# Kernel optimization log

Hardware: AMD Instinct MI355X
Metric: run time of the kernel (lower is better)

## Reference

```python
import jax, jax.numpy as jnp
import numpy as np

B, N, D, H = 16, 512, 256, 8
E_PER = 16384  # edges per graph (avg degree 32)
BN_EPS = 1e-5


def _bn(x, g, b, m, v):
    # BatchNorm1d in eval mode: normalize with running stats
    return (x - m) * (g * jax.lax.rsqrt(v + BN_EPS)) + b


def setup_inputs() -> dict:
    key = jax.random.key(0)
    ks = jax.random.split(key, 32)
    E = B * E_PER
    w = lambda k, s: (jax.random.normal(k, s, jnp.float32) * 0.02)
    # block-diagonal edge list: indices within each graph + graph offset
    src = jax.random.randint(ks[1], (B, E_PER), 0, N)
    dst = jax.random.randint(ks[2], (B, E_PER), 0, N)
    off = (jnp.arange(B) * N)[:, None]
    inp = {
        "x": jax.random.normal(ks[0], (B * N, D), jnp.float32),
        "edge_rows": (src + off).reshape(-1).astype(jnp.int32),
        "edge_cols": (dst + off).reshape(-1).astype(jnp.int32),
        "edge_vals": jax.random.uniform(ks[3], (E,), jnp.float32) * 0.1,
        "w_gcn": w(ks[4], (D, D)),
        "in_proj_w": w(ks[5], (3 * D, D)),
        "in_proj_b": w(ks[6], (3 * D,)),
        "out_proj_w": w(ks[7], (D, D)),
        "out_proj_b": w(ks[8], (D,)),
        "w1": w(ks[9], (4 * D, D)),
        "b1": w(ks[10], (4 * D,)),
        "w2": w(ks[11], (D, 4 * D)),
        "b2": w(ks[12], (D,)),
        "batch_size": B,
        "num_nodes": N,
    }
    for i, name in enumerate(["bn1", "bn2", "bn3"]):
        k4 = jax.random.split(ks[13 + i], 4)
        inp[name + "_g"] = 1.0 + jax.random.uniform(k4[0], (D,), jnp.float32) * 0.1
        inp[name + "_b"] = w(k4[1], (D,))
        inp[name + "_m"] = w(k4[2], (D,))
        inp[name + "_v"] = 1.0 + jax.random.uniform(k4[3], (D,), jnp.float32) * 0.1
    return inp


def reference(x, edge_rows, edge_cols, edge_vals, w_gcn,
              in_proj_w, in_proj_b, out_proj_w, out_proj_b,
              bn1_g, bn1_b, bn1_m, bn1_v,
              bn2_g, bn2_b, bn2_m, bn2_v,
              bn3_g, bn3_b, bn3_m, bn3_v,
              w1, b1, w2, b2, batch_size, num_nodes):
    n_total = x.shape[0]
    dh = D // H
    # --- local GCN: linear -> sparse SpMM (gather/scatter) -> exact GELU ---
    hl = x @ w_gcn.T                                            # (BN, D)
    agg = jax.ops.segment_sum(edge_vals[:, None] * hl[edge_cols],
                              edge_rows, num_segments=n_total)   # (BN, D)
    h_local = jax.nn.gelu(agg, approximate=False)
    x = x + h_local
    x = _bn(x, bn1_g, bn1_b, bn1_m, bn1_v)
    # --- global multi-head self-attention per graph ---
    h = x.reshape(batch_size, num_nodes, D)
    qkv = jnp.einsum('bnd,ed->bne', h, in_proj_w) + in_proj_b    # (B, N, 3D)
    q, k, v = jnp.split(qkv, 3, axis=-1)
    q = q.reshape(batch_size, num_nodes, H, dh)
    k = k.reshape(batch_size, num_nodes, H, dh)
    v = v.reshape(batch_size, num_nodes, H, dh)
    scores = jnp.einsum('bqhd,bkhd->bhqk', q, k) / jnp.sqrt(jnp.float32(dh))
    attn = jax.nn.softmax(scores, axis=-1)
    ctx = jnp.einsum('bhqk,bkhd->bqhd', attn, v).reshape(batch_size, num_nodes, D)
    h_attn = (ctx @ out_proj_w.T + out_proj_b).reshape(n_total, D)
    x = x + h_attn
    x = _bn(x, bn2_g, bn2_b, bn2_m, bn2_v)
    # --- FFN ---
    h_ffn = jax.nn.gelu(x @ w1.T + b1, approximate=False) @ w2.T + b2
    x = x + h_ffn
    x = _bn(x, bn3_g, bn3_b, bn3_m, bn3_v)
    return x
```

## Files before the change

### kernel.cpp

```cpp
#include <hip/hip_runtime.h>
#include <hip/hip_bf16.h>
#include <math.h>

#define D_    256
#define NT_   8192
#define NN_   512
#define B_    16
#define H_    8
#define EPG_  16384
#define BN_EPS 1e-5f

typedef __attribute__((ext_vector_type(8))) short bx8;
typedef __attribute__((ext_vector_type(4))) float fx4;

__device__ __forceinline__ float gelu_exact(float x) {
    return 0.5f * x * (1.0f + erff(x * 0.70710678118654752f));
}

typedef __attribute__((address_space(1))) const unsigned int GU;
typedef __attribute__((address_space(3))) unsigned int LU;
__device__ __forceinline__ void gl_lds16(const void* g, void* l) {
    __builtin_amdgcn_global_load_lds((GU*)g, (LU*)l, 16, 0, 0);
}

template<int TM, int TN, int EPI, int OBF, int RBF>
__global__ __launch_bounds__(256)
void mgemm(const short* __restrict__ A, const short* __restrict__ Bw,
           const float* __restrict__ bias, void* __restrict__ Cout,
           int M, int N, int K,
           long sA, long sB, long sC, long sR,
           const void* __restrict__ resid,
           const float* __restrict__ bng, const float* __restrict__ bnb,
           const float* __restrict__ bnm, const float* __restrict__ bnv)
{
    constexpr int MR = TM / 32, NR = TN / 32;
    constexpr int NIA = TM / 8, NIB = TN / 8;
    __shared__ short As[2][TM][64];
    __shared__ short Bs[2][TN][64];
    const int bz = blockIdx.z;
    A  += (size_t)bz * sA;
    Bw += (size_t)bz * sB;
    const int bm = blockIdx.y * TM, bn = blockIdx.x * TN;
    const int tid = threadIdx.x;
    const int w = tid >> 6, lane = tid & 63;
    const int wm = w >> 1, wn = w & 1;
    const int fr = lane & 15;
    const int srow = lane >> 3;
    const int scol = (((lane & 7) ^ (srow & 7)) << 3);
    fx4 acc[MR][NR] = {};

    auto STAGE = [&](int buf, int k0) {
        #pragma unroll
        for (int i = w; i < NIA + NIB; i += 4) {
            if (i < NIA)
                gl_lds16(A + (size_t)(bm + i * 8 + srow) * K + k0 + scol,
                         (char*)&As[buf][0][0] + i * 1024);
            else
                gl_lds16(Bw + (size_t)(bn + (i - NIA) * 8 + srow) * K + k0 + scol,
                         (char*)&Bs[buf][0][0] + (i - NIA) * 1024);
        }
    };

    STAGE(0, 0);
    __syncthreads();
    const int T = K >> 6;
    for (int t = 0; t < T; ++t) {
        const int cur = t & 1;
        if (t + 1 < T) STAGE(cur ^ 1, (t + 1) << 6);
        #pragma unroll
        for (int ks = 0; ks < 2; ++ks) {
            const int sl = (ks << 2) | (lane >> 4);
            bx8 af[MR], bf[NR];
            #pragma unroll
            for (int m = 0; m < MR; ++m) {
                const int row = wm * (TM / 2) + m * 16 + fr;
                af[m] = *(const bx8*)&As[cur][row][(sl ^ (row & 7)) << 3];
            }
            #pragma unroll
            for (int n = 0; n < NR; ++n) {
                const int row = wn * (TN / 2) + n * 16 + fr;
                bf[n] = *(const bx8*)&Bs[cur][row][(sl ^ (row & 7)) << 3];
            }
            #pragma unroll
            for (int m = 0; m < MR; ++m)
                #pragma unroll
                for (int n = 0; n < NR; ++n)
                    acc[m][n] = __builtin_amdgcn_mfma_f32_16x16x32_bf16(af[m], bf[n], acc[m][n], 0, 0, 0);
        }
        __syncthreads();
    }

    float* Cf = (float*)Cout + (size_t)bz * sC;
    __hip_bfloat16* Cb = (__hip_bfloat16*)Cout + (size_t)bz * sC;
    const float* Rf = (const float*)resid + (EPI >= 2 ? (size_t)bz * sR : 0);
    const __hip_bfloat16* Rb = (const __hip_bfloat16*)resid + (EPI >= 2 ? (size_t)bz * sR : 0);
    #pragma unroll
    for (int m = 0; m < MR; ++m) {
        #pragma unroll
        for (int n = 0; n < NR; ++n) {
            #pragma unroll
            for (int r = 0; r < 4; ++r) {
                const int gm = bm + wm * (TM / 2) + m * 16 + (lane >> 4) * 4 + r;
                const int gn = bn + wn * (TN / 2) + n * 16 + fr;
                float v = acc[m][n][r];
                if (bias) v += bias[gn];
                if (EPI == 1) v = gelu_exact(v);
                if (EPI == 2 || EPI == 3) {
                    const float rv = RBF ? __bfloat162float(Rb[(size_t)gm * N + gn])
                                         : Rf[(size_t)gm * N + gn];
                    if (EPI == 2) v += rv;
                    else          v = rv + gelu_exact(v);
                    v = (v - bnm[gn]) * (bng[gn] * rsqrtf(bnv[gn] + BN_EPS)) + bnb[gn];
                }
                if (OBF) Cb[(size_t)gm * N + gn] = __float2bfloat16(v);
                else     Cf[(size_t)gm * N + gn] = v;
            }
        }
    }
}

__device__ __forceinline__ void cv4(const float4 v, __hip_bfloat16* d) {
    __hip_bfloat162* dp = (__hip_bfloat162*)d;
    dp[0] = __hip_bfloat162(__float2bfloat16(v.x), __float2bfloat16(v.y));
    dp[1] = __hip_bfloat162(__float2bfloat16(v.z), __float2bfloat16(v.w));
}

__global__ __launch_bounds__(256)
void conv6(const float* __restrict__ x,  const float* __restrict__ wg,
           const float* __restrict__ iw, const float* __restrict__ ow,
           const float* __restrict__ w1, const float* __restrict__ w2,
           __hip_bfloat16* xb, __hip_bfloat16* wgb, __hip_bfloat16* iwb,
           __hip_bfloat16* owb, __hip_bfloat16* w1b, __hip_bfloat16* w2b)
{
    int i = blockIdx.x * 256 + threadIdx.x;
    const float* s; __hip_bfloat16* d; int o;
    if      (i < 524288) { s = x;  d = xb;  o = i; }
    else if (i < 540672) { s = wg; d = wgb; o = i - 524288; }
    else if (i < 589824) { s = iw; d = iwb; o = i - 540672; }
    else if (i < 606208) { s = ow; d = owb; o = i - 589824; }
    else if (i < 671744) { s = w1; d = w1b; o = i - 606208; }
    else                 { s = w2; d = w2b; o = i - 671744; }
    cv4(((const float4*)s)[o], d + (size_t)o * 4);
}

__global__ __launch_bounds__(256)
void convA(const float* __restrict__ s, __hip_bfloat16* __restrict__ d, int n4)
{
    int i = blockIdx.x * 256 + threadIdx.x;
    if (i >= n4) return;
    cv4(((const float4*)s)[i], d + (size_t)i * 4);
}

__global__ __launch_bounds__(256)
void build_S(const int* __restrict__ rows, const int* __restrict__ cols,
             const float* __restrict__ vals, float* __restrict__ SA)
{
    const int e = blockIdx.x * 256 + threadIdx.x;
    const int r = rows[e], c = cols[e];
    const int g = r >> 9;
    atomicAdd(&SA[((size_t)g << 18) + (size_t)(r & 511) * 512 + (c - (g << 9))], vals[e]);
}

__global__ __launch_bounds__(256)
void transp(const __hip_bfloat16* __restrict__ hl, __hip_bfloat16* __restrict__ hlB)
{
    __shared__ short T[64][72];
    const int nt = blockIdx.x, it = blockIdx.y, g = blockIdx.z;
    const int r0 = threadIdx.x >> 3, c8 = (threadIdx.x & 7) << 3;
    #pragma unroll
    for (int u = 0; u < 2; ++u) {
        const int r = r0 + u * 32;
        *(bx8*)&T[r][c8] = *(const bx8*)&hl[(size_t)(g * 512 + it * 64 + r) * 256 + nt * 64 + c8];
    }
    __syncthreads();
    #pragma unroll
    for (int u = 0; u < 2; ++u) {
        const int r = r0 + u * 32;
        bx8 o;
        #pragma unroll
        for (int j = 0; j < 8; ++j) o[j] = T[c8 + j][r];
        *(bx8*)&hlB[((size_t)(g * 256 + nt * 64 + r)) * 512 + it * 64 + c8] = o;
    }
}

__global__ __launch_bounds__(256, 1)
void attn_mfma(const short* __restrict__ qkv, __hip_bfloat16* __restrict__ ctx)
{
    const int swz = (blockIdx.x & 7) * 128 + (blockIdx.x >> 3);
    const int qt = swz & 7;
    const int h  = (swz >> 3) & 7;
    const int b  = swz >> 6;
    __shared__ short Ks[512][40];
    __shared__ short Vt[32][520];
    __shared__ short Ps[64][520];
    const int tid = threadIdx.x;
    const int lane = tid & 63, wq = tid >> 6;
    const short* base = qkv + (size_t)b * NN_ * 768;

    {
        const int d0 = (tid & 3) << 3;
        const int k0 = tid >> 2;
        #pragma unroll
        for (int rep = 0; rep < 8; ++rep) {
            const int key = k0 + rep * 64;
            *(bx8*)&Ks[key][d0] =
                *(const bx8*)(base + (size_t)key * 768 + 256 + h * 32 + d0);
        }
    }
    {
        const int d0 = (tid >> 6) << 3;
        const int k0 = tid & 63;
        #pragma unroll
        for (int rep = 0; rep < 8; ++rep) {
            const int key = k0 + rep * 64;
            bx8 vv = *(const bx8*)(base + (size_t)key * 768 + 512 + h * 32 + d0);
            #pragma unroll
            for (int j = 0; j < 8; ++j) Vt[d0 + j][key] = vv[j];
        }
    }
    const int fr = lane & 15, fk = (lane >> 4) << 3;
    const int qrow = qt * 64 + wq * 16 + fr;
    bx8 qf = *(const bx8*)(base + (size_t)qrow * 768 + h * 32 + fk);
    __syncthreads();

    fx4 sc[32];
    #pragma unroll
    for (int nt = 0; nt < 32; ++nt) {
        bx8 kf = *(const bx8*)&Ks[nt * 16 + fr][fk];
        fx4 z = {0.f, 0.f, 0.f, 0.f};
        sc[nt] = __builtin_amdgcn_mfma_f32_16x16x32_bf16(qf, kf, z, 0, 0, 0);
    }

    const float scale = 0.17677669529663687f;
    #pragma unroll
    for (int r = 0; r < 4; ++r) {
        float m = -1e30f;
        #pragma unroll
        for (int nt = 0; nt < 32; ++nt) m = fmaxf(m, sc[nt][r]);
        #pragma unroll
        for (int off = 1; off < 16; off <<= 1)
            m = fmaxf(m, __shfl_xor(m, off, 64));
        const float M = m * scale;
        float s = 0.f;
        #pragma unroll
        for (int nt = 0; nt < 32; ++nt) {
            const float p = __expf(sc[nt][r] * scale - M);
            sc[nt][r] = p;
            s += p;
        }
        #pragma unroll
        for (int off = 1; off < 16; off <<= 1) s += __shfl_xor(s, off, 64);
        const float inv = 1.0f / s;
        const int q = wq * 16 + (lane >> 4) * 4 + r;
        #pragma unroll
        for (int nt = 0; nt < 32; ++nt)
            *(__hip_bfloat16*)&Ps[q][nt * 16 + fr] = __float2bfloat16(sc[nt][r] * inv);
    }

    fx4 oacc[2] = {};
    #pragma unroll
    for (int step = 0; step < 16; ++step) {
        bx8 pf = *(const bx8*)&Ps[wq * 16 + fr][step * 32 + fk];
        #pragma unroll
        for (int nt = 0; nt < 2; ++nt) {
            bx8 vf = *(const bx8*)&Vt[nt * 16 + fr][step * 32 + fk];
            oacc[nt] = __builtin_amdgcn_mfma_f32_16x16x32_bf16(pf, vf, oacc[nt], 0, 0, 0);
        }
    }
    #pragma unroll
    for (int nt = 0; nt < 2; ++nt) {
        #pragma unroll
        for (int r = 0; r < 4; ++r) {
            const int q = qt * 64 + wq * 16 + (lane >> 4) * 4 + r;
            const int d = nt * 16 + fr;
            ctx[(size_t)(b * NN_ + q) * D_ + h * 32 + d] = __float2bfloat16(oacc[nt][r]);
        }
    }
}

extern "C" void kernel_launch(void* const* d_in, const int* in_sizes, int n_in,
                              void* d_out, int out_size, void* d_ws, size_t ws_size,
                              hipStream_t stream) {
    const float* x      = (const float*)d_in[0];
    const int*   erows  = (const int*)d_in[1];
    const int*   ecols  = (const int*)d_in[2];
    const float* evals  = (const float*)d_in[3];
    const float* w_gcn  = (const float*)d_in[4];
    const float* in_w   = (const float*)d_in[5];
    const float* in_b   = (const float*)d_in[6];
    const float* outw   = (const float*)d_in[7];
    const float* outb   = (const float*)d_in[8];
    const float* w1     = (const float*)d_in[9];
    const float* b1     = (const float*)d_in[10];
    const float* w2     = (const float*)d_in[11];
    const float* b2     = (const float*)d_in[12];
    const float* bn1g = (const float*)d_in[15], *bn1b = (const float*)d_in[16];
    const float* bn1m = (const float*)d_in[17], *bn1v = (const float*)d_in[18];
    const float* bn2g = (const float*)d_in[19], *bn2b = (const float*)d_in[20];
    const float* bn2m = (const float*)d_in[21], *bn2v = (const float*)d_in[22];
    const float* bn3g = (const float*)d_in[23], *bn3b = (const float*)d_in[24];
    const float* bn3m = (const float*)d_in[25], *bn3v = (const float*)d_in[26];

    short* wsS = (short*)d_ws;
    __hip_bfloat16* xb    = (__hip_bfloat16*)(wsS + 0);
    __hip_bfloat16* wgcnb = (__hip_bfloat16*)(wsS + 2097152);
    __hip_bfloat16* iwb   = (__hip_bfloat16*)(wsS + 2162688);
    __hip_bfloat16* owb   = (__hip_bfloat16*)(wsS + 2359296);
    __hip_bfloat16* w1b   = (__hip_bfloat16*)(wsS + 2424832);
    __hip_bfloat16* w2b   = (__hip_bfloat16*)(wsS + 2686976);
    short* hl   = wsS + 2949120;
    short* hlB  = wsS + 5046272;
    short* x1b  = wsS + 7143424;
    short* ctxb = wsS + 9240576;
    short* x2b  = wsS + 11337728;
    short* h1b  = wsS + 13434880;
    short* SAb  = wsS + 21823488;
    float* SA   = (float*)(wsS + 26017792);
    short* qkvb = wsS + 26017792;
    float* out  = (float*)d_out;

    dim3 blk(256);
    conv6<<<dim3(2880), blk, 0, stream>>>(x, w_gcn, in_w, outw, w1, w2,
                                          xb, wgcnb, iwb, owb, w1b, w2b);
    hipMemsetAsync(SA, 0, (size_t)16 * 512 * 512 * 4, stream);
    build_S<<<dim3(1024), blk, 0, stream>>>(erows, ecols, evals, SA);
    convA<<<dim3(4096), blk, 0, stream>>>(SA, (__hip_bfloat16*)SAb, 1048576);
    mgemm<64,64,0,1,0><<<dim3(4, 128), blk, 0, stream>>>((const short*)xb, (const short*)wgcnb,
        nullptr, hl, NT_, D_, D_, 0,0,0,0, nullptr, nullptr, nullptr, nullptr, nullptr);
    transp<<<dim3(4, 8, 16), blk, 0, stream>>>((const __hip_bfloat16*)hl, (__hip_bfloat16*)hlB);
    mgemm<64,64,3,1,0><<<dim3(4, 8, 16), blk, 0, stream>>>(SAb, hlB, nullptr, x1b,
        512, D_, 512, 262144, 131072, 131072, 131072,
        x, bn1g, bn1b, bn1m, bn1v);
    mgemm<64,64,0,1,0><<<dim3(12, 128), blk, 0, stream>>>(x1b, (const short*)iwb, in_b, qkvb,
        NT_, 3 * D_, D_, 0,0,0,0, nullptr, nullptr, nullptr, nullptr, nullptr);
    attn_mfma<<<dim3(1024), blk, 0, stream>>>(qkvb, (__hip_bfloat16*)ctxb);
    mgemm<64,64,2,1,1><<<dim3(4, 128), blk, 0, stream>>>(ctxb, (const short*)owb, outb, x2b,
        NT_, D_, D_, 0,0,0,0, x1b, bn2g, bn2b, bn2m, bn2v);
    mgemm<64,64,1,1,0><<<dim3(16, 128), blk, 0, stream>>>(x2b, (const short*)w1b, b1, h1b,
        NT_, 4 * D_, D_, 0,0,0,0, nullptr, nullptr, nullptr, nullptr, nullptr);
    mgemm<64,64,2,0,1><<<dim3(4, 128), blk, 0, stream>>>(h1b, (const short*)w2b, b2, out,
        NT_, D_, 4 * D_, 0,0,0,0, x2b, bn3g, bn3b, bn3m, bn3v);
}
```

Baseline: 246.7 us.

## Fuse transposed stores into GEMM epilogues and streamline attention softmax

Adds an EPI==4 GEMM epilogue that writes a column range directly in transposed (per-graph, feature-major) bf16 layout. This removes the separate transpose kernel for the GCN hidden features and also pre-transposes V during the QKV projection. Attention can then load Vt with contiguous vector loads instead of scattered LDS writes. The attention kernel also swaps the MFMA operands so each lane holds one query row, which cuts the softmax shuffle reductions to two steps and lets P be stored as packed 4-element vectors. The cost is strided 8-byte global stores in the GEMM epilogue for the transposed part.

```diff
diff --git a/kernel.cpp b/kernel.cpp
--- a/kernel.cpp
+++ b/kernel.cpp
@@ -11,10 +11,15 @@
 #define BN_EPS 1e-5f
 
 typedef __attribute__((ext_vector_type(8))) short bx8;
+typedef __attribute__((ext_vector_type(4))) short sx4;
 typedef __attribute__((ext_vector_type(4))) float fx4;
 
 __device__ __forceinline__ float gelu_exact(float x) {
     return 0.5f * x * (1.0f + erff(x * 0.70710678118654752f));
+}
+__device__ __forceinline__ short bf16s(float v) {
+    __hip_bfloat16 hb = __float2bfloat16(v);
+    return *(short*)&hb;
 }
 
 typedef __attribute__((address_space(1))) const unsigned int GU;
@@ -92,16 +97,18 @@
 
     float* Cf = (float*)Cout + (size_t)bz * sC;
     __hip_bfloat16* Cb = (__hip_bfloat16*)Cout + (size_t)bz * sC;
-    const float* Rf = (const float*)resid + (EPI >= 2 ? (size_t)bz * sR : 0);
-    const __hip_bfloat16* Rb = (const __hip_bfloat16*)resid + (EPI >= 2 ? (size_t)bz * sR : 0);
+    const float* Rf = (const float*)resid + ((EPI == 2 || EPI == 3) ? (size_t)bz * sR : 0);
+    const __hip_bfloat16* Rb = (const __hip_bfloat16*)resid + ((EPI == 2 || EPI == 3) ? (size_t)bz * sR : 0);
     #pragma unroll
     for (int m = 0; m < MR; ++m) {
         #pragma unroll
         for (int n = 0; n < NR; ++n) {
+            const int gm0 = bm + wm * (TM / 2) + m * 16 + (lane >> 4) * 4;
+            const int gn  = bn + wn * (TN / 2) + n * 16 + fr;
+            float vv[4];
             #pragma unroll
             for (int r = 0; r < 4; ++r) {
-                const int gm = bm + wm * (TM / 2) + m * 16 + (lane >> 4) * 4 + r;
-                const int gn = bn + wn * (TN / 2) + n * 16 + fr;
+                const int gm = gm0 + r;
                 float v = acc[m][n][r];
                 if (bias) v += bias[gn];
                 if (EPI == 1) v = gelu_exact(v);
@@ -112,8 +119,27 @@
                     else          v = rv + gelu_exact(v);
                     v = (v - bnm[gn]) * (bng[gn] * rsqrtf(bnv[gn] + BN_EPS)) + bnb[gn];
                 }
-                if (OBF) Cb[(size_t)gm * N + gn] = __float2bfloat16(v);
-                else     Cf[(size_t)gm * N + gn] = v;
+                vv[r] = v;
+            }
+            if (EPI == 4) {
+                const int tc = (int)sR;
+                if (gn >= tc) {
+                    short* Tout = (short*)resid;
+                    sx4 pk;
+                    #pragma unroll
+                    for (int r = 0; r < 4; ++r) pk[r] = bf16s(vv[r]);
+                    *(sx4*)(Tout + ((size_t)((gm0 >> 9) * (N - tc) + (gn - tc))) * 512 + (gm0 & 511)) = pk;
+                } else {
+                    #pragma unroll
+                    for (int r = 0; r < 4; ++r)
+                        Cb[(size_t)(gm0 + r) * N + gn] = __float2bfloat16(vv[r]);
+                }
+            } else {
+                #pragma unroll
+                for (int r = 0; r < 4; ++r) {
+                    if (OBF) Cb[(size_t)(gm0 + r) * N + gn] = __float2bfloat16(vv[r]);
+                    else     Cf[(size_t)(gm0 + r) * N + gn] = vv[r];
+                }
             }
         }
     }
@@ -161,30 +187,9 @@
     atomicAdd(&SA[((size_t)g << 18) + (size_t)(r & 511) * 512 + (c - (g << 9))], vals[e]);
 }
 
-__global__ __launch_bounds__(256)
-void transp(const __hip_bfloat16* __restrict__ hl, __hip_bfloat16* __restrict__ hlB)
-{
-    __shared__ short T[64][72];
-    const int nt = blockIdx.x, it = blockIdx.y, g = blockIdx.z;
-    const int r0 = threadIdx.x >> 3, c8 = (threadIdx.x & 7) << 3;
-    #pragma unroll
-    for (int u = 0; u < 2; ++u) {
-        const int r = r0 + u * 32;
-        *(bx8*)&T[r][c8] = *(const bx8*)&hl[(size_t)(g * 512 + it * 64 + r) * 256 + nt * 64 + c8];
-    }
-    __syncthreads();
-    #pragma unroll
-    for (int u = 0; u < 2; ++u) {
-        const int r = r0 + u * 32;
-        bx8 o;
-        #pragma unroll
-        for (int j = 0; j < 8; ++j) o[j] = T[c8 + j][r];
-        *(bx8*)&hlB[((size_t)(g * 256 + nt * 64 + r)) * 512 + it * 64 + c8] = o;
-    }
-}
-
 __global__ __launch_bounds__(256, 1)
-void attn_mfma(const short* __restrict__ qkv, __hip_bfloat16* __restrict__ ctx)
+void attn_mfma(const short* __restrict__ qkv, const short* __restrict__ VtG,
+               __hip_bfloat16* __restrict__ ctx)
 {
     const int swz = (blockIdx.x & 7) * 128 + (blockIdx.x >> 3);
     const int qt = swz & 7;
@@ -196,6 +201,7 @@
     const int tid = threadIdx.x;
     const int lane = tid & 63, wq = tid >> 6;
     const short* base = qkv + (size_t)b * NN_ * 768;
+    const short* vtb  = VtG + (size_t)(b * 8 + h) * 32 * 512;
 
     {
         const int d0 = (tid & 3) << 3;
@@ -208,14 +214,11 @@
         }
     }
     {
-        const int d0 = (tid >> 6) << 3;
-        const int k0 = tid & 63;
+        const int d = tid >> 3, c0 = (tid & 7) << 3;
         #pragma unroll
         for (int rep = 0; rep < 8; ++rep) {
-            const int key = k0 + rep * 64;
-            bx8 vv = *(const bx8*)(base + (size_t)key * 768 + 512 + h * 32 + d0);
-            #pragma unroll
-            for (int j = 0; j < 8; ++j) Vt[d0 + j][key] = vv[j];
+            const int c = c0 + rep * 64;
+            *(bx8*)&Vt[d][c] = *(const bx8*)(vtb + (size_t)d * 512 + c);
         }
     }
     const int fr = lane & 15, fk = (lane >> 4) << 3;
@@ -228,33 +231,40 @@
     for (int nt = 0; nt < 32; ++nt) {
         bx8 kf = *(const bx8*)&Ks[nt * 16 + fr][fk];
         fx4 z = {0.f, 0.f, 0.f, 0.f};
-        sc[nt] = __builtin_amdgcn_mfma_f32_16x16x32_bf16(qf, kf, z, 0, 0, 0);
+        sc[nt] = __builtin_amdgcn_mfma_f32_16x16x32_bf16(kf, qf, z, 0, 0, 0);
     }
 
     const float scale = 0.17677669529663687f;
-    #pragma unroll
-    for (int r = 0; r < 4; ++r) {
-        float m = -1e30f;
-        #pragma unroll
-        for (int nt = 0; nt < 32; ++nt) m = fmaxf(m, sc[nt][r]);
-        #pragma unroll
-        for (int off = 1; off < 16; off <<= 1)
-            m = fmaxf(m, __shfl_xor(m, off, 64));
-        const float M = m * scale;
-        float s = 0.f;
-        #pragma unroll
-        for (int nt = 0; nt < 32; ++nt) {
+    float mx = -1e30f;
+    #pragma unroll
+    for (int nt = 0; nt < 32; ++nt)
+        mx = fmaxf(mx, fmaxf(fmaxf(sc[nt][0], sc[nt][1]), fmaxf(sc[nt][2], sc[nt][3])));
+    mx = fmaxf(mx, __shfl_xor(mx, 16, 64));
+    mx = fmaxf(mx, __shfl_xor(mx, 32, 64));
+    const float M = mx * scale;
+    float s = 0.f;
+    #pragma unroll
+    for (int nt = 0; nt < 32; ++nt) {
+        #pragma unroll
+        for (int r = 0; r < 4; ++r) {
             const float p = __expf(sc[nt][r] * scale - M);
             sc[nt][r] = p;
             s += p;
         }
-        #pragma unroll
-        for (int off = 1; off < 16; off <<= 1) s += __shfl_xor(s, off, 64);
-        const float inv = 1.0f / s;
-        const int q = wq * 16 + (lane >> 4) * 4 + r;
-        #pragma unroll
-        for (int nt = 0; nt < 32; ++nt)
-            *(__hip_bfloat16*)&Ps[q][nt * 16 + fr] = __float2bfloat16(sc[nt][r] * inv);
+    }
+    s += __shfl_xor(s, 16, 64);
+    s += __shfl_xor(s, 32, 64);
+    const float inv = 1.0f / s;
+    {
+        const int q = wq * 16 + fr;
+        const int kb = (lane >> 4) << 2;
+        #pragma unroll
+        for (int nt = 0; nt < 32; ++nt) {
+            sx4 pk;
+            #pragma unroll
+            for (int r = 0; r < 4; ++r) pk[r] = bf16s(sc[nt][r] * inv);
+            *(sx4*)&Ps[q][nt * 16 + kb] = pk;
+        }
     }
 
     fx4 oacc[2] = {};
@@ -308,7 +318,7 @@
     __hip_bfloat16* owb   = (__hip_bfloat16*)(wsS + 2359296);
     __hip_bfloat16* w1b   = (__hip_bfloat16*)(wsS + 2424832);
     __hip_bfloat16* w2b   = (__hip_bfloat16*)(wsS + 2686976);
-    short* hl   = wsS + 2949120;
+    short* VtG  = wsS + 2949120;
     short* hlB  = wsS + 5046272;
     short* x1b  = wsS + 7143424;
     short* ctxb = wsS + 9240576;
@@ -325,15 +335,14 @@
     hipMemsetAsync(SA, 0, (size_t)16 * 512 * 512 * 4, stream);
     build_S<<<dim3(1024), blk, 0, stream>>>(erows, ecols, evals, SA);
     convA<<<dim3(4096), blk, 0, stream>>>(SA, (__hip_bfloat16*)SAb, 1048576);
-    mgemm<64,64,0,1,0><<<dim3(4, 128), blk, 0, stream>>>((const short*)xb, (const short*)wgcnb,
-        nullptr, hl, NT_, D_, D_, 0,0,0,0, nullptr, nullptr, nullptr, nullptr, nullptr);
-    transp<<<dim3(4, 8, 16), blk, 0, stream>>>((const __hip_bfloat16*)hl, (__hip_bfloat16*)hlB);
+    mgemm<64,64,4,1,0><<<dim3(4, 128), blk, 0, stream>>>((const short*)xb, (const short*)wgcnb,
+        nullptr, nullptr, NT_, D_, D_, 0,0,0,0, hlB, nullptr, nullptr, nullptr, nullptr);
     mgemm<64,64,3,1,0><<<dim3(4, 8, 16), blk, 0, stream>>>(SAb, hlB, nullptr, x1b,
         512, D_, 512, 262144, 131072, 131072, 131072,
         x, bn1g, bn1b, bn1m, bn1v);
-    mgemm<64,64,0,1,0><<<dim3(12, 128), blk, 0, stream>>>(x1b, (const short*)iwb, in_b, qkvb,
-        NT_, 3 * D_, D_, 0,0,0,0, nullptr, nullptr, nullptr, nullptr, nullptr);
-    attn_mfma<<<dim3(1024), blk, 0, stream>>>(qkvb, (__hip_bfloat16*)ctxb);
+    mgemm<64,64,4,1,0><<<dim3(12, 128), blk, 0, stream>>>(x1b, (const short*)iwb, in_b, qkvb,
+        NT_, 3 * D_, D_, 0,0,0,512, VtG, nullptr, nullptr, nullptr, nullptr);
+    attn_mfma<<<dim3(1024), blk, 0, stream>>>(qkvb, VtG, (__hip_bfloat16*)ctxb);
     mgemm<64,64,2,1,1><<<dim3(4, 128), blk, 0, stream>>>(ctxb, (const short*)owb, outb, x2b,
         NT_, D_, D_, 0,0,0,0, x1b, bn2g, bn2b, bn2m, bn2v);
     mgemm<64,64,1,1,0><<<dim3(16, 128), blk, 0, stream>>>(x2b, (const short*)w1b, b1, h1b,
```

Result: faster. 230.6 us (-6.5%).
